# Kernel optimization log

Measured on AMD Instinct MI355X. Metric: run time of the kernel, lower is better.

Reference implementation:

```python
import jax, jax.numpy as jnp
import numpy as np

EPS = 1e-5

def group_norm(x, num_groups, eps=EPS):
    # x: [B, C, H, W]; no affine (matches F.group_norm with weight=None)
    B, C, H, W = x.shape
    xg = x.reshape(B, num_groups, (C // num_groups) * H * W)
    mean = jnp.mean(xg, axis=-1, keepdims=True)
    var = jnp.var(xg, axis=-1, keepdims=True)
    xg = (xg - mean) * jax.lax.rsqrt(var + eps)
    return xg.reshape(B, C, H, W)

def setup_inputs() -> dict:
    key = jax.random.key(0)
    ks = jax.random.split(key, 5)
    B, C, H, W = 32, 256, 32, 32
    # kaiming-uniform-ish scale for linear weights
    bound = 1.0 / np.sqrt(C)
    x = jax.random.normal(ks[0], (B, C, H, W), dtype=jnp.float32)
    WQ = jax.random.uniform(ks[1], (C, C), jnp.float32, -bound, bound)
    WK = jax.random.uniform(ks[2], (C, C), jnp.float32, -bound, bound)
    WV = jax.random.uniform(ks[3], (C, C), jnp.float32, -bound, bound)
    Wo = jax.random.uniform(ks[4], (C, C), jnp.float32, -bound, bound)
    z = jnp.zeros((C,), jnp.float32)
    return {"x": x, "WQ": WQ, "bQ": z, "WK": WK, "bK": z,
            "WV": WV, "bV": z, "Wo": Wo, "bo": z}

def reference(x, WQ, bQ, WK, bK, WV, bV, Wo, bo):
    B, C, H, W = x.shape
    G = min(32, C)
    h = group_norm(x, G)                      # [B,C,H,W]
    h = h.reshape(B, C, H * W).transpose(0, 2, 1)  # [B, S, C], S = H*W
    q = h @ WQ + bQ
    k = h @ WK + bK
    v = h @ WV + bV
    scale = C ** (-0.5)
    attn = jnp.einsum('bsc,btc->bst', q, k) * scale   # [B,S,S]
    attn = jax.nn.softmax(attn, axis=-1)
    o = jnp.einsum('bst,btc->bsc', attn, v)           # [B,S,C]
    o = o @ Wo + bo                                   # output Nin while in [B,S,C]
    o = o.transpose(0, 2, 1).reshape(B, C, H, W)
    return x + o
```

## Files before the change

### kernel.cpp

```cpp
#include <hip/hip_runtime.h>
#include <stdint.h>

#define BB  32
#define CC  256
#define SS  1024
#define GG  32
#define GCH 8
#define EPS 1e-5f

typedef __attribute__((ext_vector_type(8))) short short8;
typedef __attribute__((ext_vector_type(4))) float f32x4;
typedef __attribute__((ext_vector_type(16))) float f32x16;
typedef unsigned short ushort;

__device__ __forceinline__ float bf2f(ushort u){
  union { unsigned int i; float f; } v; v.i = ((unsigned int)u) << 16; return v.f;
}
__device__ __forceinline__ ushort f2bf(float f){
  union { float f; unsigned int i; } v; v.f = f;
  unsigned int r = v.i + 0x7FFFu + ((v.i >> 16) & 1u);
  return (ushort)(r >> 16);
}
__device__ __forceinline__ unsigned int cvt_pk_bf16(float lo, float hi){
  unsigned int r;
  asm("v_cvt_pk_bf16_f32 %0, %1, %2" : "=v"(r) : "v"(lo), "v"(hi));
  return r;
}

__device__ __forceinline__ int sniff_inline(const void* xp){
  const unsigned int* xw = (const unsigned int*)xp;
  const int lane = threadIdx.x & 63;
  int ok = 0;
  #pragma unroll
  for (int j = 0; j < 4; j++){
    unsigned int w = xw[lane*4 + j];
    ushort lo = (ushort)(w & 0xFFFFu);
    int e = (lo >> 7) & 0xFF;
    ok += (lo == 0 || (e >= 100 && e <= 130)) ? 1 : 0;
  }
  #pragma unroll
  for (int o = 32; o > 0; o >>= 1) ok += __shfl_down(ok, o);
  ok = __shfl(ok, 0);
  return ok > 192;
}

typedef __attribute__((address_space(3))) unsigned int lds_uint;
typedef const __attribute__((address_space(1))) unsigned int glob_uint;
__device__ __forceinline__ void ld_lds16(const void* g, void* l){
  __builtin_amdgcn_global_load_lds((glob_uint*)g, (lds_uint*)l, 16, 0, 0);
}

__global__ __launch_bounds__(256) void pre_kernel(
    const void* x,
    const void* w0, const void* w1, const void* w2, const void* w3,
    const void* b0, const void* b1, const void* b2, const void* b3,
    ushort* __restrict__ WT, float* __restrict__ biasF,
    float* __restrict__ stats)
{
  const int f = sniff_inline(x);
  const int tid = threadIdx.x;
  if (blockIdx.x < 64){
    const int id = blockIdx.x;
    const int z = id >> 4, yb = (id >> 2) & 3, xb = id & 3;
    const float scl = (z == 0) ? 0.0901684400557f : 1.0f;
    const void* wsel = z==0?w0:z==1?w1:z==2?w2:w3;
    ushort* dst = WT + (long long)z * 65536;
    __shared__ ushort t[64][65];
    const int tx = tid & 63, ty = tid >> 6;
    const int r0 = xb * 64, c0 = yb * 64;
    for (int j = 0; j < 64; j += 4){
      const int idx = (r0+ty+j)*256 + c0+tx;
      float v = f ? bf2f(((const ushort*)wsel)[idx]) : ((const float*)wsel)[idx];
      t[ty+j][tx] = f2bf(v * scl);
    }
    __syncthreads();
    for (int j = 0; j < 64; j += 4) dst[(c0+ty+j)*256 + r0+tx] = t[tx][ty+j];
    if (xb == 0 && yb == 0){
      const void* bsel = z==0?b0:z==1?b1:z==2?b2:b3;
      float bv = f ? bf2f(((const ushort*)bsel)[tid]) : ((const float*)bsel)[tid];
      biasF[z*256 + tid] = bv * scl;
    }
  } else {
    const int id = blockIdx.x - 64;
    const int g = id & 31, b = id >> 5;
    const long long base = ((long long)b * CC + g * GCH) * SS;
    float sum = 0.f, ss = 0.f;
    if (f){
      const ushort* xg = (const ushort*)x + base;
      #pragma unroll
      for (int j = 0; j < 4; j++){
        uint4 u = *(const uint4*)(xg + (j*256 + tid)*8);
        const ushort* e = (const ushort*)&u;
        #pragma unroll
        for (int i = 0; i < 8; i++){ float v = bf2f(e[i]); sum += v; ss += v*v; }
      }
    } else {
      const float* xg = (const float*)x + base;
      #pragma unroll
      for (int j = 0; j < 8; j++){
        float4 v4 = *(const float4*)(xg + (j*256 + tid)*4);
        sum += v4.x+v4.y+v4.z+v4.w;
        ss  += v4.x*v4.x+v4.y*v4.y+v4.z*v4.z+v4.w*v4.w;
      }
    }
    __shared__ float red[8];
    const int lane = tid & 63, w = tid >> 6;
    #pragma unroll
    for (int o = 32; o > 0; o >>= 1){
      sum += __shfl_down(sum, o);
      ss  += __shfl_down(ss, o);
    }
    if (lane == 0){ red[w] = sum; red[4+w] = ss; }
    __syncthreads();
    if (tid == 0){
      float s1 = red[0]+red[1]+red[2]+red[3];
      float s2 = red[4]+red[5]+red[6]+red[7];
      float mean = s1 / (float)(GCH*SS);
      float var  = s2 / (float)(GCH*SS) - mean*mean;
      const int idx = b*GG + g;
      stats[idx*2]   = mean;
      stats[idx*2+1] = rsqrtf(var + EPS);
    }
  }
}

__global__ __launch_bounds__(256) void gn_norm(const void* __restrict__ x,
                                               ushort* __restrict__ h,
                                               const float* __restrict__ stats)
{
  const int f = sniff_inline(x);
  const int c0 = blockIdx.x * 64, s0 = blockIdx.y * 64, b = blockIdx.z;
  const int tid = threadIdx.x;
  __shared__ ushort T[64][72];
  const int row = tid >> 2;
  const int qr  = tid & 3;
  const int g = (c0 + row) >> 3;
  const float mean = stats[(b*GG + g)*2];
  const float rstd = stats[(b*GG + g)*2 + 1];
  const long long xrow = ((long long)b * CC + c0 + row) * SS + s0;
  if (f){
    const ushort* xr = (const ushort*)x + xrow;
    #pragma unroll
    for (int j = 0; j < 2; j++){
      const int col = qr*16 + j*8;
      uint4 u = *(const uint4*)(xr + col);
      const ushort* e = (const ushort*)&u;
      #pragma unroll
      for (int i = 0; i < 8; i++) T[row][col+i] = f2bf((bf2f(e[i]) - mean) * rstd);
    }
  } else {
    const float* xr = (const float*)x + xrow;
    #pragma unroll
    for (int j = 0; j < 4; j++){
      const int col = qr*16 + j*4;
      float4 v4 = *(const float4*)(xr + col);
      T[row][col+0] = f2bf((v4.x - mean) * rstd);
      T[row][col+1] = f2bf((v4.y - mean) * rstd);
      T[row][col+2] = f2bf((v4.z - mean) * rstd);
      T[row][col+3] = f2bf((v4.w - mean) * rstd);
    }
  }
  __syncthreads();
  #pragma unroll
  for (int pass = 0; pass < 2; pass++){
    const int sr = pass*32 + (tid >> 3);
    const int cl = (tid & 7) * 8;
    ushort tmp[8];
    #pragma unroll
    for (int e = 0; e < 8; e++) tmp[e] = T[cl+e][sr];
    *(uint4*)(&h[((long long)b * SS + s0 + sr) * CC + c0 + cl]) = *(const uint4*)tmp;
  }
}

template<int MODE>
__global__ __launch_bounds__(256) void gemm128(
    const ushort* __restrict__ A,
    const ushort* __restrict__ BT,
    ushort* __restrict__ Cmat,
    int lda, int ldb, int ldc, int K,
    long long sA, long long sB, long long sC,
    const float* __restrict__ biasF,
    const void* __restrict__ xres,
    void* __restrict__ outp,
    ushort* __restrict__ vTp,
    long long xoff)
{
  extern __shared__ __attribute__((aligned(16))) ushort smem[];
  ushort* As = smem;
  ushort* Bs = smem + 8192;
  const int tid  = threadIdx.x;
  const int lane = tid & 63;
  const int w    = tid >> 6;
  const int wr   = w >> 1, wc = w & 1;
  const int bz   = blockIdx.z;
  const int m0 = blockIdx.x * 128;
  const int n0 = blockIdx.y * 128;

  const int rr = lane & 15;
  const int hi = lane >> 4;
  const int crow = lane >> 3;
  const int pslot = lane & 7;

  f32x4 acc[4][4] = {};

  const ushort* Ab = A + (long long)bz * sA;
  const ushort* Bb = BT + (long long)bz * sB;

  for (int k0 = 0; k0 < K; k0 += 64){
    #pragma unroll
    for (int j = 0; j < 4; j++){
      const int ck = w*4 + j;
      const int r  = ck*8 + crow;
      const int s  = pslot ^ (r & 7);
      ld_lds16(Ab + (long long)(m0 + r) * lda + k0 + s*8, &As[ck * 512]);
    }
    #pragma unroll
    for (int j = 0; j < 4; j++){
      const int ck = w*4 + j;
      const int r  = ck*8 + crow;
      const int s  = pslot ^ (r & 7);
      ld_lds16(Bb + (long long)(n0 + r) * ldb + k0 + s*8, &Bs[ck * 512]);
    }
    asm volatile("s_waitcnt vmcnt(0)" ::: "memory");
    __builtin_amdgcn_sched_barrier(0);
    __syncthreads();

    #pragma unroll
    for (int kk = 0; kk < 2; kk++){
      short8 af[4], bfr[4];
      const int lbyte = kk*64 + hi*16;
      #pragma unroll
      for (int mf = 0; mf < 4; mf++){
        const int row = wr*64 + mf*16 + rr;
        af[mf] = *(const short8*)((const char*)As + row*128 + (lbyte ^ ((row & 7) << 4)));
      }
      #pragma unroll
      for (int nf = 0; nf < 4; nf++){
        const int row = wc*64 + nf*16 + rr;
        bfr[nf] = *(const short8*)((const char*)Bs + row*128 + (lbyte ^ ((row & 7) << 4)));
      }
      #pragma unroll
      for (int mf = 0; mf < 4; mf++)
        #pragma unroll
        for (int nf = 0; nf < 4; nf++)
          acc[mf][nf] = __builtin_amdgcn_mfma_f32_16x16x32_bf16(af[mf], bfr[nf], acc[mf][nf], 0, 0, 0);
    }
    __syncthreads();
  }

  const int rb = 4 * (lane >> 4);
  if (MODE == 0){
    if (bz < 2){
      ushort* Co = Cmat + (long long)bz * sC;
      #pragma unroll
      for (int mf = 0; mf < 4; mf++){
        #pragma unroll
        for (int nf = 0; nf < 4; nf++){
          const int col = n0 + wc*64 + nf*16 + rr;
          const float badd = biasF[bz*256 + col];
          #pragma unroll
          for (int r = 0; r < 4; r++){
            const int row = m0 + wr*64 + mf*16 + rb + r;
            Co[(long long)row * ldc + col] = f2bf(acc[mf][nf][r] + badd);
          }
        }
      }
    } else {
      #pragma unroll
      for (int mf = 0; mf < 4; mf++){
        #pragma unroll
        for (int nf = 0; nf < 4; nf++){
          const int colL = wc*64 + nf*16 + rr;
          const float badd = biasF[512 + n0 + colL];
          #pragma unroll
          for (int r = 0; r < 4; r++){
            const int rowL = wr*64 + mf*16 + rb + r;
            smem[colL * 128 + rowL] = f2bf(acc[mf][nf][r] + badd);
          }
        }
      }
      __syncthreads();
      const int bL = m0 >> 10;
      const int s0 = m0 & 1023;
      for (int i = tid; i < 2048; i += 256){
        const int colL = i >> 4;
        const int rowL = (i & 15) * 8;
        uint4 pv = *(const uint4*)(&smem[colL * 128 + rowL]);
        *(uint4*)(&vTp[((long long)bL * CC + n0 + colL) * SS + s0 + rowL]) = pv;
      }
    }
  } else {
    const int bL = m0 >> 10;
    const int s0 = m0 & 1023;
    #pragma unroll
    for (int mf = 0; mf < 4; mf++){
      #pragma unroll
      for (int nf = 0; nf < 4; nf++){
        const int colL = wc*64 + nf*16 + rr;
        const float badd = biasF[768 + n0 + colL];
        #pragma unroll
        for (int r = 0; r < 4; r++){
          const int rowL = wr*64 + mf*16 + rb + r;
          smem[colL * 128 + rowL] = f2bf(acc[mf][nf][r] + badd);
        }
      }
    }
    __syncthreads();
    const int f = sniff_inline(xres);
    for (int i = tid; i < 2048; i += 256){
      const int colL = i >> 4;
      const int rowL = (i & 15) * 8;
      const long long oi = xoff + ((long long)bL * CC + n0 + colL) * SS + s0 + rowL;
      const ushort* pu = &smem[colL * 128 + rowL];
      if (f){
        const ushort* xu = (const ushort*)xres + oi;
        ushort* ou = (ushort*)outp + oi;
        ushort tmp[8];
        #pragma unroll
        for (int e = 0; e < 8; e++) tmp[e] = f2bf(bf2f(xu[e]) + bf2f(pu[e]));
        *(uint4*)ou = *(const uint4*)tmp;
      } else {
        const float* xf = (const float*)xres + oi;
        float* of = (float*)outp + oi;
        float4 a0 = *(const float4*)xf;
        float4 a1 = *(const float4*)(xf + 4);
        float4 r0, r1;
        r0.x = a0.x + bf2f(pu[0]); r0.y = a0.y + bf2f(pu[1]);
        r0.z = a0.z + bf2f(pu[2]); r0.w = a0.w + bf2f(pu[3]);
        r1.x = a1.x + bf2f(pu[4]); r1.y = a1.y + bf2f(pu[5]);
        r1.z = a1.z + bf2f(pu[6]); r1.w = a1.w + bf2f(pu[7]);
        *(float4*)of = r0;
        *(float4*)(of + 4) = r1;
      }
    }
  }
}

__global__ __launch_bounds__(512, 1) void attn_fused(
    const ushort* __restrict__ q, const ushort* __restrict__ k,
    const ushort* __restrict__ vT, ushort* __restrict__ oC)
{
  __shared__ ushort Kb[2][64 * 256];
  __shared__ ushort Vb[2][256 * 64];
  __shared__ float  Mb[8][32];
  __shared__ float  Lb[8][32];
  const int tid = threadIdx.x, lane = tid & 63, w = tid >> 6;
  const int l31 = lane & 31, hi2 = lane >> 5;
  const int qg = w & 3, ch = w >> 2;
  const int b = blockIdx.x, qt = blockIdx.y;

  const char* kgB = (const char*)(k + (long long)b * SS * CC);
  const char* vgB = (const char*)(vT + (long long)b * CC * SS);
  const int qrow = qt*128 + qg*32 + l31;
  const ushort* qgp = q + ((long long)b * SS + qrow) * CC + hi2*8;
  ushort* ogq = oC + ((long long)b * SS + qrow) * CC;

  short8 qf[16];
  #pragma unroll
  for (int kk = 0; kk < 16; kk++)
    qf[kk] = *(const short8*)(qgp + kk*16);

  f32x16 Oa[8] = {};
  float mrow = -1e30f, lrow = 0.0f;

  #define STAGE(buf, t0)                                                        \
  {                                                                             \
    _Pragma("unroll")                                                           \
    for (int j = 0; j < 4; j++){                                                \
      const int ck = j*8 + w;                                                   \
      const int tr = ck*2 + (lane >> 5);                                        \
      const int xb = ((lane & 31) * 16) ^ ((tr & 31) << 4);                     \
      ld_lds16(kgB + (long long)((t0) + tr) * 512 + xb, &Kb[buf][ck * 512]);    \
    }                                                                           \
    _Pragma("unroll")                                                           \
    for (int j = 0; j < 4; j++){                                                \
      const int ck = j*8 + w;                                                   \
      const int vr = ck*2 + (lane >> 5);                                        \
      const int u  = (lane & 31) ^ ((vr & 7) << 2);                             \
      const int vc = vr*4 + (u & 3);                                            \
      const int tb = (u >> 2) * 16;                                             \
      ld_lds16(vgB + (long long)vc * 2048 + (t0)*2 + tb, &Vb[buf][ck * 512]);   \
    }                                                                           \
  }

  STAGE(0, 0);
  asm volatile("s_waitcnt vmcnt(0)" ::: "memory");
  __builtin_amdgcn_sched_barrier(0);
  __syncthreads();

  const int coff = hi2 * 16;
  const int kswz = l31 << 4;
  const int krow = ch*32 + l31;

  for (int t = 0; t < 16; t++){
    const int cur = t & 1;
    if (t < 15) STAGE(cur ^ 1, (t+1)*64);

    f32x16 Sa = {};
    #pragma unroll
    for (int kk = 0; kk < 16; kk++){
      const int off = kk*32 + coff;
      short8 ka = *(const short8*)((const char*)&Kb[cur][0] + krow*512 + (off ^ kswz));
      Sa = __builtin_amdgcn_mfma_f32_32x32x16_bf16(ka, qf[kk], Sa, 0, 0, 0);
    }

    float mx = Sa[0];
    #pragma unroll
    for (int r = 1; r < 16; r++) mx = fmaxf(mx, Sa[r]);
    mx = fmaxf(mx, __shfl_xor(mx, 32));
    if (!__all(mx <= mrow + 8.0f)){
      const float mn = fmaxf(mrow, mx);
      const float sc = __builtin_amdgcn_exp2f(mrow - mn);
      mrow = mn;
      lrow *= sc;
      #pragma unroll
      for (int nf = 0; nf < 8; nf++)
        #pragma unroll
        for (int r = 0; r < 16; r++) Oa[nf][r] *= sc;
    }
    float rs = 0.0f;
    #pragma unroll
    for (int r = 0; r < 16; r++){
      Sa[r] = __builtin_amdgcn_exp2f(Sa[r] - mrow); rs += Sa[r];
    }
    rs += __shfl_xor(rs, 32);
    lrow += rs;

    #pragma unroll
    for (int g = 0; g < 2; g++){
      unsigned int b0 = cvt_pk_bf16(Sa[g*8+0], Sa[g*8+1]);
      unsigned int b1 = cvt_pk_bf16(Sa[g*8+2], Sa[g*8+3]);
      unsigned int b2 = cvt_pk_bf16(Sa[g*8+4], Sa[g*8+5]);
      unsigned int b3 = cvt_pk_bf16(Sa[g*8+6], Sa[g*8+7]);
      unsigned int s0 = (unsigned int)__shfl_xor((int)b0, 32);
      unsigned int s1 = (unsigned int)__shfl_xor((int)b1, 32);
      unsigned int s2 = (unsigned int)__shfl_xor((int)b2, 32);
      unsigned int s3 = (unsigned int)__shfl_xor((int)b3, 32);
      union { uint4 u; short8 s; } pw;
      pw.u.x = hi2 ? s2 : b0;
      pw.u.y = hi2 ? s3 : b1;
      pw.u.z = hi2 ? b2 : s0;
      pw.u.w = hi2 ? b3 : s1;
      const short8 pb = pw.s;
      const int G = ch*4 + g*2 + hi2;
      #pragma unroll
      for (int nf = 0; nf < 8; nf++){
        const int c = nf*32 + l31;
        const int vr = c >> 2;
        const int slot = (((G << 2) | (c & 3)) ^ ((vr & 7) << 2));
        short8 va = *(const short8*)((const char*)&Vb[cur][0] + vr*512 + slot*16);
        Oa[nf] = __builtin_amdgcn_mfma_f32_32x32x16_bf16(va, pb, Oa[nf], 0, 0, 0);
      }
    }

    asm volatile("s_waitcnt vmcnt(0)" ::: "memory");
    __builtin_amdgcn_sched_barrier(0);
    __syncthreads();
  }
  #undef STAGE

  float* Ob = (qg < 2) ? (float*)&Kb[qg][0] : (float*)&Vb[qg - 2][0];
  if (ch == 1){
    #pragma unroll
    for (int nf = 0; nf < 8; nf++){
      #pragma unroll
      for (int r = 0; r < 16; r++){
        const int c = nf*32 + (r & 3) + 8*(r >> 2) + 4*hi2;
        Ob[c*32 + l31] = Oa[nf][r];
      }
    }
    if (hi2 == 0){ Mb[w][l31] = mrow; Lb[w][l31] = lrow; }
  }
  __syncthreads();
  if (ch == 0){
    const float m2 = Mb[w + 4][l31], l2 = Lb[w + 4][l31];
    const float mx = fmaxf(mrow, m2);
    const float f1 = __builtin_amdgcn_exp2f(mrow - mx);
    const float f2 = __builtin_amdgcn_exp2f(m2 - mx);
    const float inv = 1.0f / (f1*lrow + f2*l2);
    const float a1 = f1 * inv, a2 = f2 * inv;
    #pragma unroll
    for (int nf = 0; nf < 8; nf++){
      #pragma unroll
      for (int g = 0; g < 4; g++){
        float o0 = Oa[nf][g*4+0]*a1 + Ob[(nf*32 + g*8 + hi2*4 + 0)*32 + l31]*a2;
        float o1 = Oa[nf][g*4+1]*a1 + Ob[(nf*32 + g*8 + hi2*4 + 1)*32 + l31]*a2;
        float o2 = Oa[nf][g*4+2]*a1 + Ob[(nf*32 + g*8 + hi2*4 + 2)*32 + l31]*a2;
        float o3 = Oa[nf][g*4+3]*a1 + Ob[(nf*32 + g*8 + hi2*4 + 3)*32 + l31]*a2;
        uint2 ov;
        ov.x = cvt_pk_bf16(o0, o1);
        ov.y = cvt_pk_bf16(o2, o3);
        *(uint2*)(ogq + nf*32 + g*8 + hi2*4) = ov;
      }
    }
  }
}

extern "C" void kernel_launch(void* const* d_in, const int* in_sizes, int n_in,
                              void* d_out, int out_size, void* d_ws, size_t ws_size,
                              hipStream_t stream)
{
  (void)in_sizes; (void)n_in; (void)out_size;
  const void* x  = d_in[0];
  const void* WQ = d_in[1];
  const void* bQ = d_in[2];
  const void* WK = d_in[3];
  const void* bK = d_in[4];
  const void* WV = d_in[5];
  const void* bV = d_in[6];
  const void* Wo = d_in[7];
  const void* bo = d_in[8];

  const long long NE  = (long long)BB * SS * CC;
  const long long SC  = (long long)SS * CC;

  uint8_t* base = (uint8_t*)d_ws;
  float* biasF       = (float*)(base + 256);
  float* stats       = (float*)(base + 256 + 4096);
  ushort* WT         = (ushort*)(base + 256 + 4096 + 8192);
  ushort* h          = WT + 4 * 65536;

  const long long fixedB = 256 + 4096 + 8192 + 4LL*65536*2 + NE*2;
  int CB = 1;
  for (int c = 32; c >= 1; c >>= 1){
    if (fixedB + 4LL * c * SC * 2 <= (long long)ws_size){ CB = c; break; }
  }

  ushort* q  = h + NE;
  ushort* k  = q + (long long)CB * SC;
  ushort* vT = k + (long long)CB * SC;
  ushort* oC = vT + (long long)CB * SC;

  dim3 blk(256);
  const size_t shmem = 32768;

  pre_kernel<<<dim3(64 + GG*BB), blk, 0, stream>>>(x, WQ, WK, WV, Wo, bQ, bK, bV, bo, WT, biasF, stats);
  gn_norm<<<dim3(4, 16, BB), blk, 0, stream>>>(x, h, stats);

  for (int c0 = 0; c0 < BB; c0 += CB){
    const ushort* hC = h + (long long)c0 * SC;
    gemm128<0><<<dim3(CB*8, 2, 3), blk, shmem, stream>>>(
        hC, WT, q, CC, CC, CC, CC,
        0LL, 65536LL, (long long)CB * SC,
        biasF, nullptr, nullptr, vT, 0LL);
    attn_fused<<<dim3(CB, 8), dim3(512), 0, stream>>>(q, k, vT, oC);
    gemm128<3><<<dim3(CB*8, 2, 1), blk, shmem, stream>>>(
        oC, WT + 3*65536, nullptr, CC, CC, SS, CC,
        0LL, 0LL, 0LL,
        biasF, x, d_out, nullptr, (long long)c0 * SC);
  }
}
```

Measured before the change: 135.5 us.

## Widen QKV GEMM tile to full N and coalesce Q/K stores via LDS

Replaces the generic templated GEMM with two specialized kernels. The QKV projection now computes a 128x256 tile per block, covering all output columns, so each block loads its A tile once instead of twice. Q/K results are transposed through LDS and written as 16-byte vectors instead of scattered 2-byte stores. The output projection drops the per-chunk x/out offset (xoff), so results would be written to the wrong place if the workspace forces more than one batch chunk. Larger LDS use and more accumulators per thread may reduce occupancy.

```diff
diff --git a/kernel.cpp b/kernel.cpp
--- a/kernel.cpp
+++ b/kernel.cpp
@@ -172,18 +172,119 @@
   }
 }
 
-template<int MODE>
-__global__ __launch_bounds__(256) void gemm128(
+__global__ __launch_bounds__(256) void gemm_qkv(
+    const ushort* __restrict__ A,
+    const ushort* __restrict__ WT,
+    ushort* __restrict__ qk,
+    ushort* __restrict__ vTp,
+    long long sC,
+    const float* __restrict__ biasF)
+{
+  extern __shared__ __attribute__((aligned(16))) ushort smem[];
+  ushort* As = smem;
+  ushort* Bs = smem + 8192;
+  const int tid  = threadIdx.x;
+  const int lane = tid & 63;
+  const int w    = tid >> 6;
+  const int z    = blockIdx.y;
+  const int m0   = blockIdx.x * 128;
+
+  const int rr = lane & 15;
+  const int hi = lane >> 4;
+  const int crow = lane >> 3;
+  const int pslot = lane & 7;
+
+  f32x4 acc[2][16] = {};
+
+  const ushort* Bb = WT + (long long)z * 65536;
+
+  for (int k0 = 0; k0 < 256; k0 += 64){
+    #pragma unroll
+    for (int j = 0; j < 4; j++){
+      const int ck = w*4 + j;
+      const int r  = ck*8 + crow;
+      const int s  = pslot ^ (r & 7);
+      ld_lds16(A + (long long)(m0 + r) * CC + k0 + s*8, &As[ck * 512]);
+    }
+    #pragma unroll
+    for (int j = 0; j < 8; j++){
+      const int ck = w*8 + j;
+      const int r  = ck*8 + crow;
+      const int s  = pslot ^ (r & 7);
+      ld_lds16(Bb + (long long)r * CC + k0 + s*8, &Bs[ck * 512]);
+    }
+    asm volatile("s_waitcnt vmcnt(0)" ::: "memory");
+    __builtin_amdgcn_sched_barrier(0);
+    __syncthreads();
+
+    #pragma unroll
+    for (int kk = 0; kk < 2; kk++){
+      const int lbyte = kk*64 + hi*16;
+      short8 af[2];
+      #pragma unroll
+      for (int mf = 0; mf < 2; mf++){
+        const int row = w*32 + mf*16 + rr;
+        af[mf] = *(const short8*)((const char*)As + row*128 + (lbyte ^ ((row & 7) << 4)));
+      }
+      #pragma unroll
+      for (int nf = 0; nf < 16; nf++){
+        const int row = nf*16 + rr;
+        short8 bf = *(const short8*)((const char*)Bs + row*128 + (lbyte ^ ((row & 7) << 4)));
+        acc[0][nf] = __builtin_amdgcn_mfma_f32_16x16x32_bf16(af[0], bf, acc[0][nf], 0, 0, 0);
+        acc[1][nf] = __builtin_amdgcn_mfma_f32_16x16x32_bf16(af[1], bf, acc[1][nf], 0, 0, 0);
+      }
+    }
+    __syncthreads();
+  }
+
+  const int rb = 4 * (lane >> 4);
+  const int bL = m0 >> 10;
+  const int s0 = m0 & 1023;
+  #pragma unroll
+  for (int hN = 0; hN < 2; hN++){
+    #pragma unroll
+    for (int mf = 0; mf < 2; mf++){
+      #pragma unroll
+      for (int nf = 0; nf < 8; nf++){
+        const int gnf = hN*8 + nf;
+        const int colL = nf*16 + rr;
+        const float badd = biasF[z*256 + hN*128 + colL];
+        #pragma unroll
+        for (int r = 0; r < 4; r++){
+          const int rowL = w*32 + mf*16 + rb + r;
+          Bs[colL * 128 + rowL] = f2bf(acc[mf][gnf][r] + badd);
+        }
+      }
+    }
+    __syncthreads();
+    if (z < 2){
+      ushort* Co = qk + (long long)z * sC;
+      for (int i = tid; i < 2048; i += 256){
+        const int rowL = i >> 4;
+        const int colL = (i & 15) * 8;
+        ushort tmp[8];
+        #pragma unroll
+        for (int e = 0; e < 8; e++) tmp[e] = Bs[(colL + e) * 128 + rowL];
+        *(uint4*)(&Co[(long long)(m0 + rowL) * CC + hN*128 + colL]) = *(const uint4*)tmp;
+      }
+    } else {
+      for (int i = tid; i < 2048; i += 256){
+        const int colL = i >> 4;
+        const int rowL = (i & 15) * 8;
+        uint4 pv = *(const uint4*)(&Bs[colL * 128 + rowL]);
+        *(uint4*)(&vTp[((long long)bL * CC + hN*128 + colL) * SS + s0 + rowL]) = pv;
+      }
+    }
+    __syncthreads();
+  }
+}
+
+__global__ __launch_bounds__(256) void gemm_proj(
     const ushort* __restrict__ A,
     const ushort* __restrict__ BT,
-    ushort* __restrict__ Cmat,
-    int lda, int ldb, int ldc, int K,
-    long long sA, long long sB, long long sC,
     const float* __restrict__ biasF,
     const void* __restrict__ xres,
-    void* __restrict__ outp,
-    ushort* __restrict__ vTp,
-    long long xoff)
+    void* __restrict__ outp)
 {
   extern __shared__ __attribute__((aligned(16))) ushort smem[];
   ushort* As = smem;
@@ -192,7 +293,6 @@
   const int lane = tid & 63;
   const int w    = tid >> 6;
   const int wr   = w >> 1, wc = w & 1;
-  const int bz   = blockIdx.z;
   const int m0 = blockIdx.x * 128;
   const int n0 = blockIdx.y * 128;
 
@@ -203,23 +303,20 @@
 
   f32x4 acc[4][4] = {};
 
-  const ushort* Ab = A + (long long)bz * sA;
-  const ushort* Bb = BT + (long long)bz * sB;
-
-  for (int k0 = 0; k0 < K; k0 += 64){
+  for (int k0 = 0; k0 < 256; k0 += 64){
     #pragma unroll
     for (int j = 0; j < 4; j++){
       const int ck = w*4 + j;
       const int r  = ck*8 + crow;
       const int s  = pslot ^ (r & 7);
-      ld_lds16(Ab + (long long)(m0 + r) * lda + k0 + s*8, &As[ck * 512]);
+      ld_lds16(A + (long long)(m0 + r) * CC + k0 + s*8, &As[ck * 512]);
     }
     #pragma unroll
     for (int j = 0; j < 4; j++){
       const int ck = w*4 + j;
       const int r  = ck*8 + crow;
       const int s  = pslot ^ (r & 7);
-      ld_lds16(Bb + (long long)(n0 + r) * ldb + k0 + s*8, &Bs[ck * 512]);
+      ld_lds16(BT + (long long)(n0 + r) * CC + k0 + s*8, &Bs[ck * 512]);
     }
     asm volatile("s_waitcnt vmcnt(0)" ::: "memory");
     __builtin_amdgcn_sched_barrier(0);
@@ -249,89 +346,47 @@
   }
 
   const int rb = 4 * (lane >> 4);
-  if (MODE == 0){
-    if (bz < 2){
-      ushort* Co = Cmat + (long long)bz * sC;
-      #pragma unroll
-      for (int mf = 0; mf < 4; mf++){
-        #pragma unroll
-        for (int nf = 0; nf < 4; nf++){
-          const int col = n0 + wc*64 + nf*16 + rr;
-          const float badd = biasF[bz*256 + col];
-          #pragma unroll
-          for (int r = 0; r < 4; r++){
-            const int row = m0 + wr*64 + mf*16 + rb + r;
-            Co[(long long)row * ldc + col] = f2bf(acc[mf][nf][r] + badd);
-          }
-        }
-      }
+  const int bL = m0 >> 10;
+  const int s0 = m0 & 1023;
+  #pragma unroll
+  for (int mf = 0; mf < 4; mf++){
+    #pragma unroll
+    for (int nf = 0; nf < 4; nf++){
+      const int colL = wc*64 + nf*16 + rr;
+      const float badd = biasF[768 + n0 + colL];
+      #pragma unroll
+      for (int r = 0; r < 4; r++){
+        const int rowL = wr*64 + mf*16 + rb + r;
+        smem[colL * 128 + rowL] = f2bf(acc[mf][nf][r] + badd);
+      }
+    }
+  }
+  __syncthreads();
+  const int f = sniff_inline(xres);
+  for (int i = tid; i < 2048; i += 256){
+    const int colL = i >> 4;
+    const int rowL = (i & 15) * 8;
+    const long long oi = ((long long)bL * CC + n0 + colL) * SS + s0 + rowL;
+    const ushort* pu = &smem[colL * 128 + rowL];
+    if (f){
+      const ushort* xu = (const ushort*)xres + oi;
+      ushort* ou = (ushort*)outp + oi;
+      ushort tmp[8];
+      #pragma unroll
+      for (int e = 0; e < 8; e++) tmp[e] = f2bf(bf2f(xu[e]) + bf2f(pu[e]));
+      *(uint4*)ou = *(const uint4*)tmp;
     } else {
-      #pragma unroll
-      for (int mf = 0; mf < 4; mf++){
-        #pragma unroll
-        for (int nf = 0; nf < 4; nf++){
-          const int colL = wc*64 + nf*16 + rr;
-          const float badd = biasF[512 + n0 + colL];
-          #pragma unroll
-          for (int r = 0; r < 4; r++){
-            const int rowL = wr*64 + mf*16 + rb + r;
-            smem[colL * 128 + rowL] = f2bf(acc[mf][nf][r] + badd);
-          }
-        }
-      }
-      __syncthreads();
-      const int bL = m0 >> 10;
-      const int s0 = m0 & 1023;
-      for (int i = tid; i < 2048; i += 256){
-        const int colL = i >> 4;
-        const int rowL = (i & 15) * 8;
-        uint4 pv = *(const uint4*)(&smem[colL * 128 + rowL]);
-        *(uint4*)(&vTp[((long long)bL * CC + n0 + colL) * SS + s0 + rowL]) = pv;
-      }
-    }
-  } else {
-    const int bL = m0 >> 10;
-    const int s0 = m0 & 1023;
-    #pragma unroll
-    for (int mf = 0; mf < 4; mf++){
-      #pragma unroll
-      for (int nf = 0; nf < 4; nf++){
-        const int colL = wc*64 + nf*16 + rr;
-        const float badd = biasF[768 + n0 + colL];
-        #pragma unroll
-        for (int r = 0; r < 4; r++){
-          const int rowL = wr*64 + mf*16 + rb + r;
-          smem[colL * 128 + rowL] = f2bf(acc[mf][nf][r] + badd);
-        }
-      }
-    }
-    __syncthreads();
-    const int f = sniff_inline(xres);
-    for (int i = tid; i < 2048; i += 256){
-      const int colL = i >> 4;
-      const int rowL = (i & 15) * 8;
-      const long long oi = xoff + ((long long)bL * CC + n0 + colL) * SS + s0 + rowL;
-      const ushort* pu = &smem[colL * 128 + rowL];
-      if (f){
-        const ushort* xu = (const ushort*)xres + oi;
-        ushort* ou = (ushort*)outp + oi;
-        ushort tmp[8];
-        #pragma unroll
-        for (int e = 0; e < 8; e++) tmp[e] = f2bf(bf2f(xu[e]) + bf2f(pu[e]));
-        *(uint4*)ou = *(const uint4*)tmp;
-      } else {
-        const float* xf = (const float*)xres + oi;
-        float* of = (float*)outp + oi;
-        float4 a0 = *(const float4*)xf;
-        float4 a1 = *(const float4*)(xf + 4);
-        float4 r0, r1;
-        r0.x = a0.x + bf2f(pu[0]); r0.y = a0.y + bf2f(pu[1]);
-        r0.z = a0.z + bf2f(pu[2]); r0.w = a0.w + bf2f(pu[3]);
-        r1.x = a1.x + bf2f(pu[4]); r1.y = a1.y + bf2f(pu[5]);
-        r1.z = a1.z + bf2f(pu[6]); r1.w = a1.w + bf2f(pu[7]);
-        *(float4*)of = r0;
-        *(float4*)(of + 4) = r1;
-      }
+      const float* xf = (const float*)xres + oi;
+      float* of = (float*)outp + oi;
+      float4 a0 = *(const float4*)xf;
+      float4 a1 = *(const float4*)(xf + 4);
+      float4 r0, r1;
+      r0.x = a0.x + bf2f(pu[0]); r0.y = a0.y + bf2f(pu[1]);
+      r0.z = a0.z + bf2f(pu[2]); r0.w = a0.w + bf2f(pu[3]);
+      r1.x = a1.x + bf2f(pu[4]); r1.y = a1.y + bf2f(pu[5]);
+      r1.z = a1.z + bf2f(pu[6]); r1.w = a1.w + bf2f(pu[7]);
+      *(float4*)of = r0;
+      *(float4*)(of + 4) = r1;
     }
   }
 }
@@ -532,21 +587,17 @@
   ushort* oC = vT + (long long)CB * SC;
 
   dim3 blk(256);
-  const size_t shmem = 32768;
+  const size_t shmem = 49152;
 
   pre_kernel<<<dim3(64 + GG*BB), blk, 0, stream>>>(x, WQ, WK, WV, Wo, bQ, bK, bV, bo, WT, biasF, stats);
   gn_norm<<<dim3(4, 16, BB), blk, 0, stream>>>(x, h, stats);
 
   for (int c0 = 0; c0 < BB; c0 += CB){
     const ushort* hC = h + (long long)c0 * SC;
-    gemm128<0><<<dim3(CB*8, 2, 3), blk, shmem, stream>>>(
-        hC, WT, q, CC, CC, CC, CC,
-        0LL, 65536LL, (long long)CB * SC,
-        biasF, nullptr, nullptr, vT, 0LL);
+    gemm_qkv<<<dim3(CB*8, 3), blk, shmem, stream>>>(
+        hC, WT, q, vT, (long long)CB * SC, biasF);
     attn_fused<<<dim3(CB, 8), dim3(512), 0, stream>>>(q, k, vT, oC);
-    gemm128<3><<<dim3(CB*8, 2, 1), blk, shmem, stream>>>(
-        oC, WT + 3*65536, nullptr, CC, CC, SS, CC,
-        0LL, 0LL, 0LL,
-        biasF, x, d_out, nullptr, (long long)c0 * SC);
-  }
-}
+    gemm_proj<<<dim3(CB*8, 2), blk, shmem, stream>>>(
+        oC, WT + 3*65536, biasF, x, d_out);
+  }
+}
```

New measurement: 167.0 us. 1.23x slower.

## Single-buffer K/V tiles in attention kernel and split epilogue merge into rounds

Applied to the files above, without the earlier changes.

Removes double buffering of the K and V shared-memory tiles, so each iteration loads its tile and waits before computing. Shared memory per block is roughly halved. The cross-wave output merge is now done in two rounds so the smaller buffers can hold the partial outputs. The launch bound stays at one block per CU, so the smaller footprint may not raise occupancy, and the global load latency is no longer overlapped with MFMA work.

```diff
diff --git a/kernel.cpp b/kernel.cpp
--- a/kernel.cpp
+++ b/kernel.cpp
@@ -340,8 +340,8 @@
     const ushort* __restrict__ q, const ushort* __restrict__ k,
     const ushort* __restrict__ vT, ushort* __restrict__ oC)
 {
-  __shared__ ushort Kb[2][64 * 256];
-  __shared__ ushort Vb[2][256 * 64];
+  __shared__ ushort Kb[64 * 256];
+  __shared__ ushort Vb[256 * 64];
   __shared__ float  Mb[8][32];
   __shared__ float  Lb[8][32];
   const int tid = threadIdx.x, lane = tid & 63, w = tid >> 6;
@@ -363,14 +363,14 @@
   f32x16 Oa[8] = {};
   float mrow = -1e30f, lrow = 0.0f;
 
-  #define STAGE(buf, t0)                                                        \
+  #define STAGE(t0)                                                             \
   {                                                                             \
     _Pragma("unroll")                                                           \
     for (int j = 0; j < 4; j++){                                                \
       const int ck = j*8 + w;                                                   \
       const int tr = ck*2 + (lane >> 5);                                        \
       const int xb = ((lane & 31) * 16) ^ ((tr & 31) << 4);                     \
-      ld_lds16(kgB + (long long)((t0) + tr) * 512 + xb, &Kb[buf][ck * 512]);    \
+      ld_lds16(kgB + (long long)((t0) + tr) * 512 + xb, &Kb[ck * 512]);         \
     }                                                                           \
     _Pragma("unroll")                                                           \
     for (int j = 0; j < 4; j++){                                                \
@@ -379,28 +379,25 @@
       const int u  = (lane & 31) ^ ((vr & 7) << 2);                             \
       const int vc = vr*4 + (u & 3);                                            \
       const int tb = (u >> 2) * 16;                                             \
-      ld_lds16(vgB + (long long)vc * 2048 + (t0)*2 + tb, &Vb[buf][ck * 512]);   \
+      ld_lds16(vgB + (long long)vc * 2048 + (t0)*2 + tb, &Vb[ck * 512]);        \
     }                                                                           \
   }
-
-  STAGE(0, 0);
-  asm volatile("s_waitcnt vmcnt(0)" ::: "memory");
-  __builtin_amdgcn_sched_barrier(0);
-  __syncthreads();
 
   const int coff = hi2 * 16;
   const int kswz = l31 << 4;
   const int krow = ch*32 + l31;
 
   for (int t = 0; t < 16; t++){
-    const int cur = t & 1;
-    if (t < 15) STAGE(cur ^ 1, (t+1)*64);
+    STAGE(t*64);
+    asm volatile("s_waitcnt vmcnt(0)" ::: "memory");
+    __builtin_amdgcn_sched_barrier(0);
+    __syncthreads();
 
     f32x16 Sa = {};
     #pragma unroll
     for (int kk = 0; kk < 16; kk++){
       const int off = kk*32 + coff;
-      short8 ka = *(const short8*)((const char*)&Kb[cur][0] + krow*512 + (off ^ kswz));
+      short8 ka = *(const short8*)((const char*)Kb + krow*512 + (off ^ kswz));
       Sa = __builtin_amdgcn_mfma_f32_32x32x16_bf16(ka, qf[kk], Sa, 0, 0, 0);
     }
 
@@ -448,51 +445,59 @@
         const int c = nf*32 + l31;
         const int vr = c >> 2;
         const int slot = (((G << 2) | (c & 3)) ^ ((vr & 7) << 2));
-        short8 va = *(const short8*)((const char*)&Vb[cur][0] + vr*512 + slot*16);
+        short8 va = *(const short8*)((const char*)Vb + vr*512 + slot*16);
         Oa[nf] = __builtin_amdgcn_mfma_f32_32x32x16_bf16(va, pb, Oa[nf], 0, 0, 0);
       }
     }
 
-    asm volatile("s_waitcnt vmcnt(0)" ::: "memory");
-    __builtin_amdgcn_sched_barrier(0);
     __syncthreads();
   }
   #undef STAGE
 
-  float* Ob = (qg < 2) ? (float*)&Kb[qg][0] : (float*)&Vb[qg - 2][0];
-  if (ch == 1){
-    #pragma unroll
-    for (int nf = 0; nf < 8; nf++){
-      #pragma unroll
-      for (int r = 0; r < 16; r++){
-        const int c = nf*32 + (r & 3) + 8*(r >> 2) + 4*hi2;
-        Ob[c*32 + l31] = Oa[nf][r];
-      }
-    }
-    if (hi2 == 0){ Mb[w][l31] = mrow; Lb[w][l31] = lrow; }
-  }
-  __syncthreads();
-  if (ch == 0){
-    const float m2 = Mb[w + 4][l31], l2 = Lb[w + 4][l31];
-    const float mx = fmaxf(mrow, m2);
-    const float f1 = __builtin_amdgcn_exp2f(mrow - mx);
-    const float f2 = __builtin_amdgcn_exp2f(m2 - mx);
-    const float inv = 1.0f / (f1*lrow + f2*l2);
-    const float a1 = f1 * inv, a2 = f2 * inv;
-    #pragma unroll
-    for (int nf = 0; nf < 8; nf++){
-      #pragma unroll
-      for (int g = 0; g < 4; g++){
-        float o0 = Oa[nf][g*4+0]*a1 + Ob[(nf*32 + g*8 + hi2*4 + 0)*32 + l31]*a2;
-        float o1 = Oa[nf][g*4+1]*a1 + Ob[(nf*32 + g*8 + hi2*4 + 1)*32 + l31]*a2;
-        float o2 = Oa[nf][g*4+2]*a1 + Ob[(nf*32 + g*8 + hi2*4 + 2)*32 + l31]*a2;
-        float o3 = Oa[nf][g*4+3]*a1 + Ob[(nf*32 + g*8 + hi2*4 + 3)*32 + l31]*a2;
-        uint2 ov;
-        ov.x = cvt_pk_bf16(o0, o1);
-        ov.y = cvt_pk_bf16(o2, o3);
-        *(uint2*)(ogq + nf*32 + g*8 + hi2*4) = ov;
-      }
-    }
+  float* Ob = (qg < 2) ? (float*)&Kb[(qg & 1) * 16384] : (float*)&Vb[(qg & 1) * 16384];
+  Ob = nullptr;
+  for (int round = 0; round < 2; round++){
+    float* slab = (round == 0) ? (float*)&Kb[0] : (float*)&Vb[0];
+    const int myround = qg >> 1;
+    float* myOb = ((qg & 1) == 0) ? (float*)&Kb[0] : (float*)&Vb[0];
+    (void)slab;
+    if (myround == round){
+      if (ch == 1){
+        #pragma unroll
+        for (int nf = 0; nf < 8; nf++){
+          #pragma unroll
+          for (int r = 0; r < 16; r++){
+            const int c = nf*32 + (r & 3) + 8*(r >> 2) + 4*hi2;
+            myOb[c*32 + l31] = Oa[nf][r];
+          }
+        }
+        if (hi2 == 0){ Mb[w][l31] = mrow; Lb[w][l31] = lrow; }
+      }
+    }
+    __syncthreads();
+    if (myround == round && ch == 0){
+      const float m2 = Mb[w + 4][l31], l2 = Lb[w + 4][l31];
+      const float mx = fmaxf(mrow, m2);
+      const float f1 = __builtin_amdgcn_exp2f(mrow - mx);
+      const float f2 = __builtin_amdgcn_exp2f(m2 - mx);
+      const float inv = 1.0f / (f1*lrow + f2*l2);
+      const float a1 = f1 * inv, a2 = f2 * inv;
+      #pragma unroll
+      for (int nf = 0; nf < 8; nf++){
+        #pragma unroll
+        for (int g = 0; g < 4; g++){
+          float o0 = Oa[nf][g*4+0]*a1 + myOb[(nf*32 + g*8 + hi2*4 + 0)*32 + l31]*a2;
+          float o1 = Oa[nf][g*4+1]*a1 + myOb[(nf*32 + g*8 + hi2*4 + 1)*32 + l31]*a2;
+          float o2 = Oa[nf][g*4+2]*a1 + myOb[(nf*32 + g*8 + hi2*4 + 2)*32 + l31]*a2;
+          float o3 = Oa[nf][g*4+3]*a1 + myOb[(nf*32 + g*8 + hi2*4 + 3)*32 + l31]*a2;
+          uint2 ov;
+          ov.x = cvt_pk_bf16(o0, o1);
+          ov.y = cvt_pk_bf16(o2, o3);
+          *(uint2*)(ogq + nf*32 + g*8 + hi2*4) = ov;
+        }
+      }
+    }
+    __syncthreads();
   }
 }
 
```

Result: no change. 137.6 us (+1.5%).
